# Optimization experiments

Measured on AMD Instinct MI355X. Metric: run time of the kernel, lower is better.

Reference implementation:

```python
import jax, jax.numpy as jnp
import numpy as np

DIM = 512
HID = DIM // 4        # cross-attention inner dim
MLP_HID = int(DIM * 2.0)
EPS = 1e-5


def _xavier(key, shape):
    fan_in, fan_out = shape[0], shape[1]
    limit = float(np.sqrt(6.0 / (fan_in + fan_out)))
    return jax.random.uniform(key, shape, jnp.float32, -limit, limit)


def setup_inputs() -> dict:
    key = jax.random.key(0)
    ks = jax.random.split(key, 12)
    n, v = 8, 2048
    x = jax.random.normal(ks[0], (n, v, DIM), jnp.float32)
    y = jax.random.normal(ks[1], (n, v, DIM), jnp.float32)
    Wq = _xavier(ks[2], (DIM, HID))
    Wk = _xavier(ks[3], (DIM, HID))
    Wv = _xavier(ks[4], (DIM, DIM))
    gamma = jnp.ones((DIM,), jnp.float32)
    beta = jnp.zeros((DIM,), jnp.float32)
    # nn.Linear default init: U(-1/sqrt(fan_in), 1/sqrt(fan_in))
    b1lim = 1.0 / np.sqrt(DIM)
    W1 = jax.random.uniform(ks[5], (DIM, MLP_HID), jnp.float32, -b1lim, b1lim)
    b1 = jax.random.uniform(ks[6], (MLP_HID,), jnp.float32, -b1lim, b1lim)
    b2lim = 1.0 / np.sqrt(MLP_HID)
    W2 = jax.random.uniform(ks[7], (MLP_HID, DIM), jnp.float32, -b2lim, b2lim)
    b2 = jax.random.uniform(ks[8], (DIM,), jnp.float32, -b2lim, b2lim)
    return {"x": x, "y": y, "Wq": Wq, "Wk": Wk, "Wv": Wv,
            "gamma": gamma, "beta": beta, "W1": W1, "b1": b1, "W2": W2, "b2": b2}


def _layernorm(x, gamma, beta):
    mu = jnp.mean(x, axis=-1, keepdims=True)
    var = jnp.var(x, axis=-1, keepdims=True)
    return (x - mu) * jax.lax.rsqrt(var + EPS) * gamma + beta


def reference(x, y, Wq, Wk, Wv, gamma, beta, W1, b1, W2, b2):
    scale = HID ** (-0.5)
    q = jnp.einsum('nvc,co->nvo', x, Wq)          # [n, q, HID]
    k = jnp.einsum('nvc,co->nvo', y, Wk)          # [n, k, HID]
    v = jnp.einsum('nvc,co->nvo', y, Wv)          # [n, k, DIM]
    attn = jax.nn.softmax(jnp.einsum('nqc,nkc->nqk', q, k) * scale, axis=-1)
    x = x + jnp.einsum('nqk,nkc->nqc', attn, v)   # residual + attention
    h = _layernorm(x, gamma, beta)
    h = jax.nn.gelu(h @ W1 + b1, approximate=False) @ W2 + b2
    return x + h
```

## Files before the change

### kernel.cpp

```cpp
#include <hip/hip_runtime.h>
#include <cstddef>
#include <cstdint>

typedef __attribute__((ext_vector_type(8))) short short8;
typedef __attribute__((ext_vector_type(4))) short s16x4;
typedef __attribute__((ext_vector_type(4))) float f32x4;
typedef __attribute__((ext_vector_type(16))) float f32x16;

#define GLOAD_LDS16(gp, lp) __builtin_amdgcn_global_load_lds( \
    (const __attribute__((address_space(1))) void*)(gp),      \
    (__attribute__((address_space(3))) void*)(lp), 16, 0, 0)

__device__ __forceinline__ short f2bf(float f) {
    union { float f; unsigned u; } v; v.f = f;
    unsigned r = v.u + 0x7fffu + ((v.u >> 16) & 1u);
    return (short)(r >> 16);
}

__global__ __launch_bounds__(256) void prep_kernel(
    const float* __restrict__ Wq, const float* __restrict__ Wk,
    const float* __restrict__ Wv, const float* __restrict__ W1,
    const float* __restrict__ W2,
    short* WqT, short* WkT, short* WvT, short* W1T, short* W2T)
{
    __shared__ short tile[64][68];
    int b2 = blockIdx.x;
    const float* in; short* out; int R, C;
    if (b2 < 16)       { in = Wq; out = WqT; R = 512;  C = 128; }
    else if (b2 < 32)  { in = Wk; out = WkT; R = 512;  C = 128;  b2 -= 16; }
    else if (b2 < 96)  { in = Wv; out = WvT; R = 512;  C = 512;  b2 -= 32; }
    else if (b2 < 224) { in = W1; out = W1T; R = 512;  C = 1024; b2 -= 96; }
    else               { in = W2; out = W2T; R = 1024; C = 512;  b2 -= 224; }
    int nx = C >> 6;
    int r0 = (b2 / nx) * 64, c0 = (b2 % nx) * 64;
    int t = threadIdx.x, tr = t >> 6, tc = t & 63;
#pragma unroll
    for (int i = 0; i < 16; ++i) {
        int r = i * 4 + tr;
        tile[r][tc] = f2bf(in[(size_t)(r0 + r) * C + (c0 + tc)]);
    }
    __syncthreads();
#pragma unroll
    for (int i = 0; i < 16; ++i) {
        int r = i * 4 + tr;
        out[(size_t)(c0 + r) * R + (r0 + tc)] = tile[tc][r];
    }
}

__global__ __launch_bounds__(256, 3) void proj_gemm(
    const float* __restrict__ x, const float* __restrict__ y,
    const short* __restrict__ WqT, const short* __restrict__ WkT,
    const short* __restrict__ WvT,
    short* __restrict__ qbf, short* __restrict__ kbff, short* __restrict__ vbf)
{
    __shared__ short As[128][64];
    __shared__ short Bs[128][64];
    int bid = blockIdx.x;
    const float* A; const short* BT; short* outp; int n0, N, mode, mb;
    if (bid < 128)      { A = x; BT = WqT; outp = qbf;  n0 = 0; N = 128; mode = 0; mb = bid; }
    else if (bid < 256) { A = y; BT = WkT; outp = kbff; n0 = 0; N = 128; mode = 0; mb = bid - 128; }
    else { int v2 = bid - 256; A = y; BT = WvT; outp = vbf; n0 = (v2 & 3) << 7; N = 512; mode = 1; mb = v2 >> 2; }
    const int m0 = mb << 7;
    const int K = 512;
    const int t = threadIdx.x, l = t & 63, w = t >> 6;
    const int wm = w >> 1, wn = w & 1;
    const int lo = l & 15, hi = l >> 4;

    f32x4 acc[4][4] = {};
    const int srow = l >> 3;
    const int scg  = (l & 7) ^ (srow & 7);

    for (int kt = 0; kt < K; kt += 64) {
#pragma unroll
        for (int i = 0; i < 4; ++i) {
            int seg = w * 4 + i;
            int row = seg * 8 + srow;
            GLOAD_LDS16(BT + (size_t)(n0 + row) * K + kt + scg * 8, &Bs[seg * 8][0]);
        }
#pragma unroll
        for (int i = 0; i < 4; ++i) {
            int c = i * 256 + t;
            int row = c >> 3, ch = c & 7;
            const float* src = A + (size_t)(m0 + row) * K + kt + ch * 8;
            f32x4 u0 = *(const f32x4*)src;
            f32x4 u1 = *(const f32x4*)(src + 4);
            int d0, d1, d2, d3;
            asm("v_cvt_pk_bf16_f32 %0, %1, %2" : "=v"(d0) : "v"(u0[0]), "v"(u0[1]));
            asm("v_cvt_pk_bf16_f32 %0, %1, %2" : "=v"(d1) : "v"(u0[2]), "v"(u0[3]));
            asm("v_cvt_pk_bf16_f32 %0, %1, %2" : "=v"(d2) : "v"(u1[0]), "v"(u1[1]));
            asm("v_cvt_pk_bf16_f32 %0, %1, %2" : "=v"(d3) : "v"(u1[2]), "v"(u1[3]));
            union { int i[4]; short8 v; } uu;
            uu.i[0] = d0; uu.i[1] = d1; uu.i[2] = d2; uu.i[3] = d3;
            *(short8*)&As[row][((ch ^ (row & 7)) * 8)] = uu.v;
        }
        __syncthreads();
#pragma unroll
        for (int kk = 0; kk < 2; ++kk) {
            short8 af[4], bfv[4];
            const int rc = ((kk * 4 + hi) ^ (lo & 7)) * 8;
#pragma unroll
            for (int mi = 0; mi < 4; ++mi)
                af[mi] = *(const short8*)&As[wm * 64 + mi * 16 + lo][rc];
#pragma unroll
            for (int ni = 0; ni < 4; ++ni)
                bfv[ni] = *(const short8*)&Bs[wn * 64 + ni * 16 + lo][rc];
            __builtin_amdgcn_s_setprio(1);
#pragma unroll
            for (int mi = 0; mi < 4; ++mi)
#pragma unroll
                for (int ni = 0; ni < 4; ++ni)
                    acc[mi][ni] = __builtin_amdgcn_mfma_f32_16x16x32_bf16(
                        af[mi], bfv[ni], acc[mi][ni], 0, 0, 0);
            __builtin_amdgcn_s_setprio(0);
        }
        __syncthreads();
    }

    if (mode == 0) {
#pragma unroll
        for (int mi = 0; mi < 4; ++mi) {
#pragma unroll
            for (int ni = 0; ni < 4; ++ni) {
                int rowb = m0 + wm * 64 + mi * 16 + hi * 4;
                int col  = n0 + wn * 64 + ni * 16 + lo;
                size_t base = ((size_t)(rowb >> 5) * (N >> 4) + (col >> 4)) * 512
                            + ((col & 15) >> 3) * 256 + (rowb & 31) * 8 + (col & 7);
#pragma unroll
                for (int r = 0; r < 4; ++r)
                    outp[base + r * 8] = f2bf(acc[mi][ni][r]);
            }
        }
    } else {
#pragma unroll
        for (int mi = 0; mi < 4; ++mi) {
#pragma unroll
            for (int ni = 0; ni < 4; ++ni) {
                int rowb = m0 + wm * 64 + mi * 16 + hi * 4;
                int col  = n0 + wn * 64 + ni * 16 + lo;
                size_t base = ((size_t)(rowb >> 4) * (N >> 5) + (col >> 5)) * 512
                            + ((rowb & 15) >> 3) * 256 + (col & 31) * 8 + (rowb & 7);
                s16x4 pk;
#pragma unroll
                for (int r = 0; r < 4; ++r) pk[r] = f2bf(acc[mi][ni][r]);
                *(s16x4*)(outp + base) = pk;
            }
        }
    }
}

template<int EPI>
__global__ __launch_bounds__(256, 3) void gemm_kernel(
    const short* __restrict__ A, const short* __restrict__ BT, void* outv,
    const float* __restrict__ bias, const float* __restrict__ resid,
    int N, int K)
{
    __shared__ short As[128][64];
    __shared__ short Bs[128][64];
    int bid = blockIdx.x;
    const int cpx = gridDim.x >> 3;
    bid = (bid & 7) * cpx + (bid >> 3);
    const int nb = N >> 7;
    const int m0 = (bid / nb) << 7;
    const int n0 = (bid % nb) << 7;
    const int t = threadIdx.x, l = t & 63, w = t >> 6;
    const int wm = w >> 1, wn = w & 1;
    const int lo = l & 15, hi = l >> 4;

    f32x4 acc[4][4] = {};
    const int srow = l >> 3;
    const int scg  = (l & 7) ^ (srow & 7);

    for (int kt = 0; kt < K; kt += 64) {
#pragma unroll
        for (int i = 0; i < 4; ++i) {
            int seg = w * 4 + i;
            int row = seg * 8 + srow;
            GLOAD_LDS16(A + (size_t)(m0 + row) * K + kt + scg * 8, &As[seg * 8][0]);
        }
#pragma unroll
        for (int i = 0; i < 4; ++i) {
            int seg = w * 4 + i;
            int row = seg * 8 + srow;
            GLOAD_LDS16(BT + (size_t)(n0 + row) * K + kt + scg * 8, &Bs[seg * 8][0]);
        }
        __syncthreads();
#pragma unroll
        for (int kk = 0; kk < 2; ++kk) {
            short8 af[4], bfv[4];
            const int rc = ((kk * 4 + hi) ^ (lo & 7)) * 8;
#pragma unroll
            for (int mi = 0; mi < 4; ++mi)
                af[mi] = *(const short8*)&As[wm * 64 + mi * 16 + lo][rc];
#pragma unroll
            for (int ni = 0; ni < 4; ++ni)
                bfv[ni] = *(const short8*)&Bs[wn * 64 + ni * 16 + lo][rc];
            __builtin_amdgcn_s_setprio(1);
#pragma unroll
            for (int mi = 0; mi < 4; ++mi)
#pragma unroll
                for (int ni = 0; ni < 4; ++ni)
                    acc[mi][ni] = __builtin_amdgcn_mfma_f32_16x16x32_bf16(
                        af[mi], bfv[ni], acc[mi][ni], 0, 0, 0);
            __builtin_amdgcn_s_setprio(0);
        }
        __syncthreads();
    }

#pragma unroll
    for (int mi = 0; mi < 4; ++mi) {
#pragma unroll
        for (int ni = 0; ni < 4; ++ni) {
#pragma unroll
            for (int r = 0; r < 4; ++r) {
                int row = m0 + wm * 64 + mi * 16 + hi * 4 + r;
                int col = n0 + wn * 64 + ni * 16 + lo;
                size_t idx = (size_t)row * N + col;
                float v = acc[mi][ni][r];
                if (EPI == 2) {
                    v += bias[col];
                    v = 0.5f * v * (1.0f + erff(v * 0.70710678118654752f));
                    ((short*)outv)[idx] = f2bf(v);
                } else {
                    v += bias[col] + resid[idx];
                    ((float*)outv)[idx] = v;
                }
            }
        }
    }
}

__global__ __launch_bounds__(512, 1) void flash_kernel(
    const float* __restrict__ x,
    const short* __restrict__ qbf,
    const short* __restrict__ kbff,
    const short* __restrict__ vbf,
    float* __restrict__ xres,
    const float* __restrict__ gamma,
    const float* __restrict__ beta,
    short* __restrict__ hb)
{
    __shared__ short Ps[2][2][8][512];
    __shared__ float lpart[8][32];
    __shared__ float rsum[8][64];
    __shared__ float rsq[8][64];
    __shared__ float murs[2][64];

    const int bid = blockIdx.x;
    const int n = bid & 7;
    const int qtile = bid >> 3;
    const int q0 = qtile << 6;
    const int t = threadIdx.x, l = t & 63, w = t >> 6;
    const int qh = w >> 2, kq = w & 3;
    const int lo5 = l & 31, hi2 = l >> 5;
    const float C1 = 0.08838834764831845f * 1.4426950408889634f;

    short8 qf[8];
    {
        const short* qp = qbf + (((size_t)(n * 64 + qtile * 2 + qh) * 8) << 9) + l * 8;
#pragma unroll
        for (int s = 0; s < 8; ++s) qf[s] = *(const short8*)(qp + (s << 9));
    }

    f32x16 o00 = {}, o01 = {}, o10 = {}, o11 = {};
    float lp = 0.f;

    const short* kb0 = kbff + (((size_t)(n * 64) * 8) << 9);
    const short* vb0 = vbf + ((((size_t)(n * 128)) * 16 + w * 2) << 9);

    short8 preg0, preg1;

    {
        const short* kp = kb0 + (((size_t)kq * 8) << 9) + l * 8;
        short8 kf[8];
#pragma unroll
        for (int s = 0; s < 8; ++s) kf[s] = *(const short8*)(kp + (s << 9));
        f32x16 sa = {};
        __builtin_amdgcn_s_setprio(1);
#pragma unroll
        for (int s = 0; s < 8; ++s)
            sa = __builtin_amdgcn_mfma_f32_32x32x16_bf16(kf[s], qf[s], sa, 0, 0, 0);
        __builtin_amdgcn_s_setprio(0);
        float lsum = 0.f;
#pragma unroll
        for (int r = 0; r < 16; ++r) {
            float p = exp2f(sa[r] * C1);
            sa[r] = p; lsum += p;
        }
        lp = lsum;
        int wq[8], sx[8];
#pragma unroll
        for (int q2 = 0; q2 < 8; ++q2) {
            int a;
            asm("v_cvt_pk_bf16_f32 %0, %1, %2"
                : "=v"(a) : "v"(sa[2 * q2]), "v"(sa[2 * q2 + 1]));
            wq[q2] = a;
        }
#pragma unroll
        for (int q2 = 0; q2 < 8; ++q2) sx[q2] = __shfl_xor(wq[q2], 32);
        union { int i[4]; short8 v; } u0, u1;
        u0.i[0] = hi2 ? sx[2] : wq[0];
        u0.i[1] = hi2 ? sx[3] : wq[1];
        u0.i[2] = hi2 ? wq[2] : sx[0];
        u0.i[3] = hi2 ? wq[3] : sx[1];
        u1.i[0] = hi2 ? sx[6] : wq[4];
        u1.i[1] = hi2 ? sx[7] : wq[5];
        u1.i[2] = hi2 ? wq[6] : sx[4];
        u1.i[3] = hi2 ? wq[7] : sx[5];
        *(short8*)&Ps[0][qh][kq * 2][l * 8]     = u0.v;
        *(short8*)&Ps[0][qh][kq * 2 + 1][l * 8] = u1.v;
    }

    for (int kt2 = 0; kt2 < 16; ++kt2) {
        const bool hn = kt2 < 15;
        const short* vp = vb0 + (((size_t)(kt2 * 128)) << 9) + l * 8;

        short8 kf[8];
        if (hn) {
            const short* kp = kb0 + (((size_t)((kt2 + 1) * 4 + kq) * 8) << 9) + l * 8;
#pragma unroll
            for (int s = 0; s < 8; ++s) kf[s] = *(const short8*)(kp + (s << 9));
        }
        short8 vfa[8];
#pragma unroll
        for (int p = 0; p < 8; ++p)
            vfa[p] = *(const short8*)(vp + (((size_t)((p >> 1) * 16 + (p & 1))) << 9));

        if (hn) {
            f32x16 sa = {};
            __builtin_amdgcn_s_setprio(1);
#pragma unroll
            for (int s = 0; s < 8; ++s)
                sa = __builtin_amdgcn_mfma_f32_32x32x16_bf16(kf[s], qf[s], sa, 0, 0, 0);
            __builtin_amdgcn_s_setprio(0);
            float lsum = 0.f;
#pragma unroll
            for (int r = 0; r < 16; ++r) {
                float p = exp2f(sa[r] * C1);
                sa[r] = p; lsum += p;
            }
            lp += lsum;
            int wq[8], sx[8];
#pragma unroll
            for (int q2 = 0; q2 < 8; ++q2) {
                int a;
                asm("v_cvt_pk_bf16_f32 %0, %1, %2"
                    : "=v"(a) : "v"(sa[2 * q2]), "v"(sa[2 * q2 + 1]));
                wq[q2] = a;
            }
#pragma unroll
            for (int q2 = 0; q2 < 8; ++q2) sx[q2] = __shfl_xor(wq[q2], 32);
            union { int i[4]; short8 v; } u0, u1;
            u0.i[0] = hi2 ? sx[2] : wq[0];
            u0.i[1] = hi2 ? sx[3] : wq[1];
            u0.i[2] = hi2 ? wq[2] : sx[0];
            u0.i[3] = hi2 ? wq[3] : sx[1];
            u1.i[0] = hi2 ? sx[6] : wq[4];
            u1.i[1] = hi2 ? sx[7] : wq[5];
            u1.i[2] = hi2 ? wq[6] : sx[4];
            u1.i[3] = hi2 ? wq[7] : sx[5];
            preg0 = u0.v; preg1 = u1.v;
        }

        __syncthreads();

        short8 vfb[8];
#pragma unroll
        for (int p = 0; p < 8; ++p)
            vfb[p] = *(const short8*)(vp + (((size_t)((4 + (p >> 1)) * 16 + (p & 1))) << 9));

        if (hn) {
            const int nb2 = (kt2 + 1) & 1;
            *(short8*)&Ps[nb2][qh][kq * 2][l * 8]     = preg0;
            *(short8*)&Ps[nb2][qh][kq * 2 + 1][l * 8] = preg1;
        }

        const int pb = kt2 & 1;
        __builtin_amdgcn_s_setprio(1);
#pragma unroll
        for (int ks = 0; ks < 4; ++ks) {
            short8 p0 = *(const short8*)&Ps[pb][0][ks][l * 8];
            short8 p1 = *(const short8*)&Ps[pb][1][ks][l * 8];
            o00 = __builtin_amdgcn_mfma_f32_32x32x16_bf16(p0, vfa[ks * 2 + 0], o00, 0, 0, 0);
            o01 = __builtin_amdgcn_mfma_f32_32x32x16_bf16(p0, vfa[ks * 2 + 1], o01, 0, 0, 0);
            o10 = __builtin_amdgcn_mfma_f32_32x32x16_bf16(p1, vfa[ks * 2 + 0], o10, 0, 0, 0);
            o11 = __builtin_amdgcn_mfma_f32_32x32x16_bf16(p1, vfa[ks * 2 + 1], o11, 0, 0, 0);
        }
#pragma unroll
        for (int ks = 4; ks < 8; ++ks) {
            short8 p0 = *(const short8*)&Ps[pb][0][ks][l * 8];
            short8 p1 = *(const short8*)&Ps[pb][1][ks][l * 8];
            o00 = __builtin_amdgcn_mfma_f32_32x32x16_bf16(p0, vfb[(ks - 4) * 2 + 0], o00, 0, 0, 0);
            o01 = __builtin_amdgcn_mfma_f32_32x32x16_bf16(p0, vfb[(ks - 4) * 2 + 1], o01, 0, 0, 0);
            o10 = __builtin_amdgcn_mfma_f32_32x32x16_bf16(p1, vfb[(ks - 4) * 2 + 0], o10, 0, 0, 0);
            o11 = __builtin_amdgcn_mfma_f32_32x32x16_bf16(p1, vfb[(ks - 4) * 2 + 1], o11, 0, 0, 0);
        }
        __builtin_amdgcn_s_setprio(0);
    }

    float l2 = lp + __shfl_xor(lp, 32);
    if (l < 32) lpart[w][l] = l2;
    __syncthreads();
    float li0 = 1.f / (lpart[0][lo5] + lpart[1][lo5] + lpart[2][lo5] + lpart[3][lo5]);
    float li1 = 1.f / (lpart[4][lo5] + lpart[5][lo5] + lpart[6][lo5] + lpart[7][lo5]);
    const int c0 = w * 64 + lo5;
#pragma unroll
    for (int r = 0; r < 16; ++r) {
        int qr = (r & 3) + 8 * (r >> 2) + 4 * hi2;
        float ir0 = __shfl(li0, qr);
        float ir1 = __shfl(li1, qr);
        size_t b0 = ((size_t)(n * 2048 + q0 + qr) << 9) + c0;
        size_t b1 = ((size_t)(n * 2048 + q0 + 32 + qr) << 9) + c0;
        float v00 = x[b0]      + o00[r] * ir0;
        float v01 = x[b0 + 32] + o01[r] * ir0;
        float v10 = x[b1]      + o10[r] * ir1;
        float v11 = x[b1 + 32] + o11[r] * ir1;
        xres[b0] = v00; xres[b0 + 32] = v01;
        xres[b1] = v10; xres[b1 + 32] = v11;
        o00[r] = v00; o01[r] = v01; o10[r] = v10; o11[r] = v11;
        float s0 = v00 + v01, sq0 = v00 * v00 + v01 * v01;
        float s1 = v10 + v11, sq1 = v10 * v10 + v11 * v11;
#pragma unroll
        for (int mm = 1; mm < 32; mm <<= 1) {
            s0 += __shfl_xor(s0, mm); sq0 += __shfl_xor(sq0, mm);
            s1 += __shfl_xor(s1, mm); sq1 += __shfl_xor(sq1, mm);
        }
        if (lo5 == 0) {
            rsum[w][qr] = s0;      rsq[w][qr] = sq0;
            rsum[w][32 + qr] = s1; rsq[w][32 + qr] = sq1;
        }
    }
    __syncthreads();
    if (t < 64) {
        float s = 0.f, qq = 0.f;
#pragma unroll
        for (int ww = 0; ww < 8; ++ww) { s += rsum[ww][t]; qq += rsq[ww][t]; }
        float mu = s * (1.0f / 512.0f);
        float var = qq * (1.0f / 512.0f) - mu * mu;
        murs[0][t] = mu;
        murs[1][t] = rsqrtf(var + 1e-5f);
    }
    __syncthreads();
    const float g0 = gamma[c0], g1 = gamma[c0 + 32];
    const float e0 = beta[c0],  e1 = beta[c0 + 32];
#pragma unroll
    for (int r = 0; r < 16; ++r) {
        int qr = (r & 3) + 8 * (r >> 2) + 4 * hi2;
        float mu0 = murs[0][qr],      rs0 = murs[1][qr];
        float mu1 = murs[0][32 + qr], rs1 = murs[1][32 + qr];
        size_t h0 = ((size_t)(n * 2048 + q0 + qr) << 9) + c0;
        size_t h1 = ((size_t)(n * 2048 + q0 + 32 + qr) << 9) + c0;
        hb[h0]      = f2bf((o00[r] - mu0) * rs0 * g0 + e0);
        hb[h0 + 32] = f2bf((o01[r] - mu0) * rs0 * g1 + e1);
        hb[h1]      = f2bf((o10[r] - mu1) * rs1 * g0 + e0);
        hb[h1 + 32] = f2bf((o11[r] - mu1) * rs1 * g1 + e1);
    }
}

extern "C" void kernel_launch(void* const* d_in, const int* in_sizes, int n_in,
                              void* d_out, int out_size, void* d_ws, size_t ws_size,
                              hipStream_t stream)
{
    const float* x     = (const float*)d_in[0];
    const float* y     = (const float*)d_in[1];
    const float* Wq    = (const float*)d_in[2];
    const float* Wk    = (const float*)d_in[3];
    const float* Wv    = (const float*)d_in[4];
    const float* gamma = (const float*)d_in[5];
    const float* beta  = (const float*)d_in[6];
    const float* W1    = (const float*)d_in[7];
    const float* b1    = (const float*)d_in[8];
    const float* W2    = (const float*)d_in[9];
    const float* b2    = (const float*)d_in[10];
    float* out = (float*)d_out;

    char* ws = (char*)d_ws;
    size_t off = 0;
    auto alloc = [&](size_t bytes) -> void* {
        void* p = ws + off;
        off += (bytes + 255) & ~(size_t)255;
        return p;
    };
    short* WqT  = (short*)alloc((size_t)128 * 512 * 2);
    short* WkT  = (short*)alloc((size_t)128 * 512 * 2);
    short* WvT  = (short*)alloc((size_t)512 * 512 * 2);
    short* W1T  = (short*)alloc((size_t)1024 * 512 * 2);
    short* W2T  = (short*)alloc((size_t)512 * 1024 * 2);
    short* qbf  = (short*)alloc((size_t)16384 * 128 * 2);
    short* kbff = (short*)alloc((size_t)16384 * 128 * 2);
    short* vbf  = (short*)alloc((size_t)16384 * 512 * 2);
    short* hb   = (short*)alloc((size_t)16384 * 512 * 2);
    short* gb   = (short*)alloc((size_t)16384 * 1024 * 2);

    prep_kernel<<<352, 256, 0, stream>>>(Wq, Wk, Wv, W1, W2,
                                         WqT, WkT, WvT, W1T, W2T);
    proj_gemm<<<768, 256, 0, stream>>>(x, y, WqT, WkT, WvT, qbf, kbff, vbf);
    flash_kernel<<<256, 512, 0, stream>>>(x, qbf, kbff, vbf, out, gamma, beta, hb);
    gemm_kernel<2><<<1024, 256, 0, stream>>>(hb, W1T, gb, b1, nullptr, 1024, 512);
    gemm_kernel<3><<<512,  256, 0, stream>>>(gb, W2T, out, b2, out, 512, 1024);

    (void)in_sizes; (void)n_in; (void)out_size; (void)ws_size;
}
```

Baseline: 169.0 us.

## Use 16 waves per flash block, splitting query halves across wave groups

Grows the flash attention block from 8 to 16 waves. Each group of 8 waves owns one 32-row query half and computes scores for a 256-key tile, so the loop runs 8 iterations instead of 16. Each wave now holds two output accumulators instead of four. Q and K fragments are reloaded from global memory inside the score loop instead of being kept in registers, and V is loaded in chunks. The aim is more waves in flight and less register pressure per wave, at the cost of repeated Q reads and a larger block barrier.

```diff
diff --git a/kernel.cpp b/kernel.cpp
--- a/kernel.cpp
+++ b/kernel.cpp
@@ -229,7 +229,7 @@
     }
 }
 
-__global__ __launch_bounds__(512, 1) void flash_kernel(
+__global__ __launch_bounds__(1024, 1) void flash_kernel(
     const float* __restrict__ x,
     const short* __restrict__ qbf,
     const short* __restrict__ kbff,
@@ -239,10 +239,10 @@
     const float* __restrict__ beta,
     short* __restrict__ hb)
 {
-    __shared__ short Ps[2][2][8][512];
-    __shared__ float lpart[8][32];
-    __shared__ float rsum[8][64];
-    __shared__ float rsq[8][64];
+    __shared__ short Ps[2][2][16][512];
+    __shared__ float lpart[16][32];
+    __shared__ float rsum[16][32];
+    __shared__ float rsq[16][32];
     __shared__ float murs[2][64];
 
     const int bid = blockIdx.x;
@@ -250,36 +250,26 @@
     const int qtile = bid >> 3;
     const int q0 = qtile << 6;
     const int t = threadIdx.x, l = t & 63, w = t >> 6;
-    const int qh = w >> 2, kq = w & 3;
+    const int qh = w >> 3, sub = w & 7;
     const int lo5 = l & 31, hi2 = l >> 5;
     const float C1 = 0.08838834764831845f * 1.4426950408889634f;
 
-    short8 qf[8];
+    const short* qp = qbf + (((size_t)(n * 64 + qtile * 2 + qh) * 8) << 9) + l * 8;
+    const short* kb0 = kbff + (((size_t)(n * 64) * 8) << 9);
+
+    f32x16 o0 = {}, o1 = {};
+    float lp = 0.f;
+    short8 preg0, preg1;
+
     {
-        const short* qp = qbf + (((size_t)(n * 64 + qtile * 2 + qh) * 8) << 9) + l * 8;
-#pragma unroll
-        for (int s = 0; s < 8; ++s) qf[s] = *(const short8*)(qp + (s << 9));
-    }
-
-    f32x16 o00 = {}, o01 = {}, o10 = {}, o11 = {};
-    float lp = 0.f;
-
-    const short* kb0 = kbff + (((size_t)(n * 64) * 8) << 9);
-    const short* vb0 = vbf + ((((size_t)(n * 128)) * 16 + w * 2) << 9);
-
-    short8 preg0, preg1;
-
-    {
-        const short* kp = kb0 + (((size_t)kq * 8) << 9) + l * 8;
-        short8 kf[8];
-#pragma unroll
-        for (int s = 0; s < 8; ++s) kf[s] = *(const short8*)(kp + (s << 9));
+        const short* kp = kb0 + (((size_t)(sub * 8)) << 9) + l * 8;
         f32x16 sa = {};
-        __builtin_amdgcn_s_setprio(1);
-#pragma unroll
-        for (int s = 0; s < 8; ++s)
-            sa = __builtin_amdgcn_mfma_f32_32x32x16_bf16(kf[s], qf[s], sa, 0, 0, 0);
-        __builtin_amdgcn_s_setprio(0);
+#pragma unroll
+        for (int s = 0; s < 8; ++s) {
+            short8 kf = *(const short8*)(kp + ((size_t)s << 9));
+            short8 qv = *(const short8*)(qp + ((size_t)s << 9));
+            sa = __builtin_amdgcn_mfma_f32_32x32x16_bf16(kf, qv, sa, 0, 0, 0);
+        }
         float lsum = 0.f;
 #pragma unroll
         for (int r = 0; r < 16; ++r) {
@@ -306,31 +296,23 @@
         u1.i[1] = hi2 ? sx[7] : wq[5];
         u1.i[2] = hi2 ? wq[6] : sx[4];
         u1.i[3] = hi2 ? wq[7] : sx[5];
-        *(short8*)&Ps[0][qh][kq * 2][l * 8]     = u0.v;
-        *(short8*)&Ps[0][qh][kq * 2 + 1][l * 8] = u1.v;
-    }
-
-    for (int kt2 = 0; kt2 < 16; ++kt2) {
-        const bool hn = kt2 < 15;
-        const short* vp = vb0 + (((size_t)(kt2 * 128)) << 9) + l * 8;
-
-        short8 kf[8];
+        *(short8*)&Ps[0][qh][sub * 2][l * 8]     = u0.v;
+        *(short8*)&Ps[0][qh][sub * 2 + 1][l * 8] = u1.v;
+    }
+
+    for (int kt2 = 0; kt2 < 8; ++kt2) {
+        const bool hn = kt2 < 7;
+
         if (hn) {
-            const short* kp = kb0 + (((size_t)((kt2 + 1) * 4 + kq) * 8) << 9) + l * 8;
-#pragma unroll
-            for (int s = 0; s < 8; ++s) kf[s] = *(const short8*)(kp + (s << 9));
-        }
-        short8 vfa[8];
-#pragma unroll
-        for (int p = 0; p < 8; ++p)
-            vfa[p] = *(const short8*)(vp + (((size_t)((p >> 1) * 16 + (p & 1))) << 9));
-
-        if (hn) {
+            const short* kp = kb0 + (((size_t)(((kt2 + 1) * 8 + sub) * 8)) << 9) + l * 8;
             f32x16 sa = {};
             __builtin_amdgcn_s_setprio(1);
 #pragma unroll
-            for (int s = 0; s < 8; ++s)
-                sa = __builtin_amdgcn_mfma_f32_32x32x16_bf16(kf[s], qf[s], sa, 0, 0, 0);
+            for (int s = 0; s < 8; ++s) {
+                short8 kf = *(const short8*)(kp + ((size_t)s << 9));
+                short8 qv = *(const short8*)(qp + ((size_t)s << 9));
+                sa = __builtin_amdgcn_mfma_f32_32x32x16_bf16(kf, qv, sa, 0, 0, 0);
+            }
             __builtin_amdgcn_s_setprio(0);
             float lsum = 0.f;
 #pragma unroll
@@ -363,77 +345,68 @@
 
         __syncthreads();
 
-        short8 vfb[8];
-#pragma unroll
-        for (int p = 0; p < 8; ++p)
-            vfb[p] = *(const short8*)(vp + (((size_t)((4 + (p >> 1)) * 16 + (p & 1))) << 9));
-
         if (hn) {
             const int nb2 = (kt2 + 1) & 1;
-            *(short8*)&Ps[nb2][qh][kq * 2][l * 8]     = preg0;
-            *(short8*)&Ps[nb2][qh][kq * 2 + 1][l * 8] = preg1;
+            *(short8*)&Ps[nb2][qh][sub * 2][l * 8]     = preg0;
+            *(short8*)&Ps[nb2][qh][sub * 2 + 1][l * 8] = preg1;
         }
 
         const int pb = kt2 & 1;
-        __builtin_amdgcn_s_setprio(1);
-#pragma unroll
-        for (int ks = 0; ks < 4; ++ks) {
-            short8 p0 = *(const short8*)&Ps[pb][0][ks][l * 8];
-            short8 p1 = *(const short8*)&Ps[pb][1][ks][l * 8];
-            o00 = __builtin_amdgcn_mfma_f32_32x32x16_bf16(p0, vfa[ks * 2 + 0], o00, 0, 0, 0);
-            o01 = __builtin_amdgcn_mfma_f32_32x32x16_bf16(p0, vfa[ks * 2 + 1], o01, 0, 0, 0);
-            o10 = __builtin_amdgcn_mfma_f32_32x32x16_bf16(p1, vfa[ks * 2 + 0], o10, 0, 0, 0);
-            o11 = __builtin_amdgcn_mfma_f32_32x32x16_bf16(p1, vfa[ks * 2 + 1], o11, 0, 0, 0);
-        }
-#pragma unroll
-        for (int ks = 4; ks < 8; ++ks) {
-            short8 p0 = *(const short8*)&Ps[pb][0][ks][l * 8];
-            short8 p1 = *(const short8*)&Ps[pb][1][ks][l * 8];
-            o00 = __builtin_amdgcn_mfma_f32_32x32x16_bf16(p0, vfb[(ks - 4) * 2 + 0], o00, 0, 0, 0);
-            o01 = __builtin_amdgcn_mfma_f32_32x32x16_bf16(p0, vfb[(ks - 4) * 2 + 1], o01, 0, 0, 0);
-            o10 = __builtin_amdgcn_mfma_f32_32x32x16_bf16(p1, vfb[(ks - 4) * 2 + 0], o10, 0, 0, 0);
-            o11 = __builtin_amdgcn_mfma_f32_32x32x16_bf16(p1, vfb[(ks - 4) * 2 + 1], o11, 0, 0, 0);
-        }
-        __builtin_amdgcn_s_setprio(0);
+        const short* vp = vbf + ((((size_t)(n * 128 + kt2 * 16) * 16) + sub * 2) << 9) + l * 8;
+#pragma unroll
+        for (int ch = 0; ch < 4; ++ch) {
+            short8 pa[4], vf[8];
+#pragma unroll
+            for (int j = 0; j < 4; ++j) {
+                int ks = ch * 4 + j;
+                pa[j]         = *(const short8*)&Ps[pb][qh][ks][l * 8];
+                vf[j * 2]     = *(const short8*)(vp + (((size_t)(ks * 16)) << 9));
+                vf[j * 2 + 1] = *(const short8*)(vp + (((size_t)(ks * 16 + 1)) << 9));
+            }
+            __builtin_amdgcn_s_setprio(1);
+#pragma unroll
+            for (int j = 0; j < 4; ++j) {
+                o0 = __builtin_amdgcn_mfma_f32_32x32x16_bf16(pa[j], vf[j * 2],     o0, 0, 0, 0);
+                o1 = __builtin_amdgcn_mfma_f32_32x32x16_bf16(pa[j], vf[j * 2 + 1], o1, 0, 0, 0);
+            }
+            __builtin_amdgcn_s_setprio(0);
+        }
     }
 
     float l2 = lp + __shfl_xor(lp, 32);
     if (l < 32) lpart[w][l] = l2;
     __syncthreads();
-    float li0 = 1.f / (lpart[0][lo5] + lpart[1][lo5] + lpart[2][lo5] + lpart[3][lo5]);
-    float li1 = 1.f / (lpart[4][lo5] + lpart[5][lo5] + lpart[6][lo5] + lpart[7][lo5]);
-    const int c0 = w * 64 + lo5;
+    float li;
+    {
+        const int b0 = qh * 8;
+        li = 1.f / (lpart[b0][lo5] + lpart[b0 + 1][lo5] + lpart[b0 + 2][lo5] +
+                    lpart[b0 + 3][lo5] + lpart[b0 + 4][lo5] + lpart[b0 + 5][lo5] +
+                    lpart[b0 + 6][lo5] + lpart[b0 + 7][lo5]);
+    }
+    const int c0 = sub * 64 + lo5;
 #pragma unroll
     for (int r = 0; r < 16; ++r) {
         int qr = (r & 3) + 8 * (r >> 2) + 4 * hi2;
-        float ir0 = __shfl(li0, qr);
-        float ir1 = __shfl(li1, qr);
-        size_t b0 = ((size_t)(n * 2048 + q0 + qr) << 9) + c0;
-        size_t b1 = ((size_t)(n * 2048 + q0 + 32 + qr) << 9) + c0;
-        float v00 = x[b0]      + o00[r] * ir0;
-        float v01 = x[b0 + 32] + o01[r] * ir0;
-        float v10 = x[b1]      + o10[r] * ir1;
-        float v11 = x[b1 + 32] + o11[r] * ir1;
-        xres[b0] = v00; xres[b0 + 32] = v01;
-        xres[b1] = v10; xres[b1 + 32] = v11;
-        o00[r] = v00; o01[r] = v01; o10[r] = v10; o11[r] = v11;
-        float s0 = v00 + v01, sq0 = v00 * v00 + v01 * v01;
-        float s1 = v10 + v11, sq1 = v10 * v10 + v11 * v11;
+        float ir = __shfl(li, qr);
+        size_t base = ((size_t)(n * 2048 + q0 + qh * 32 + qr) << 9) + c0;
+        float v0 = x[base]      + o0[r] * ir;
+        float v1 = x[base + 32] + o1[r] * ir;
+        xres[base] = v0; xres[base + 32] = v1;
+        o0[r] = v0; o1[r] = v1;
+        float s = v0 + v1;
+        float sq = v0 * v0 + v1 * v1;
 #pragma unroll
         for (int mm = 1; mm < 32; mm <<= 1) {
-            s0 += __shfl_xor(s0, mm); sq0 += __shfl_xor(sq0, mm);
-            s1 += __shfl_xor(s1, mm); sq1 += __shfl_xor(sq1, mm);
-        }
-        if (lo5 == 0) {
-            rsum[w][qr] = s0;      rsq[w][qr] = sq0;
-            rsum[w][32 + qr] = s1; rsq[w][32 + qr] = sq1;
-        }
+            s += __shfl_xor(s, mm); sq += __shfl_xor(sq, mm);
+        }
+        if (lo5 == 0) { rsum[w][qr] = s; rsq[w][qr] = sq; }
     }
     __syncthreads();
     if (t < 64) {
+        const int bq = (t >> 5) * 8, qr = t & 31;
         float s = 0.f, qq = 0.f;
 #pragma unroll
-        for (int ww = 0; ww < 8; ++ww) { s += rsum[ww][t]; qq += rsq[ww][t]; }
+        for (int k = 0; k < 8; ++k) { s += rsum[bq + k][qr]; qq += rsq[bq + k][qr]; }
         float mu = s * (1.0f / 512.0f);
         float var = qq * (1.0f / 512.0f) - mu * mu;
         murs[0][t] = mu;
@@ -445,14 +418,10 @@
 #pragma unroll
     for (int r = 0; r < 16; ++r) {
         int qr = (r & 3) + 8 * (r >> 2) + 4 * hi2;
-        float mu0 = murs[0][qr],      rs0 = murs[1][qr];
-        float mu1 = murs[0][32 + qr], rs1 = murs[1][32 + qr];
-        size_t h0 = ((size_t)(n * 2048 + q0 + qr) << 9) + c0;
-        size_t h1 = ((size_t)(n * 2048 + q0 + 32 + qr) << 9) + c0;
-        hb[h0]      = f2bf((o00[r] - mu0) * rs0 * g0 + e0);
-        hb[h0 + 32] = f2bf((o01[r] - mu0) * rs0 * g1 + e1);
-        hb[h1]      = f2bf((o10[r] - mu1) * rs1 * g0 + e0);
-        hb[h1 + 32] = f2bf((o11[r] - mu1) * rs1 * g1 + e1);
+        float mu = murs[0][qh * 32 + qr], rs = murs[1][qh * 32 + qr];
+        size_t base = ((size_t)(n * 2048 + q0 + qh * 32 + qr) << 9) + c0;
+        hb[base]      = f2bf((o0[r] - mu) * rs * g0 + e0);
+        hb[base + 32] = f2bf((o1[r] - mu) * rs * g1 + e1);
     }
 }
 
@@ -494,7 +463,7 @@
     prep_kernel<<<352, 256, 0, stream>>>(Wq, Wk, Wv, W1, W2,
                                          WqT, WkT, WvT, W1T, W2T);
     proj_gemm<<<768, 256, 0, stream>>>(x, y, WqT, WkT, WvT, qbf, kbff, vbf);
-    flash_kernel<<<256, 512, 0, stream>>>(x, qbf, kbff, vbf, out, gamma, beta, hb);
+    flash_kernel<<<256, 1024, 0, stream>>>(x, qbf, kbff, vbf, out, gamma, beta, hb);
     gemm_kernel<2><<<1024, 256, 0, stream>>>(hb, W1T, gb, b1, nullptr, 1024, 512);
     gemm_kernel<3><<<512,  256, 0, stream>>>(gb, W2T, out, b2, out, 512, 1024);
 
```

After: 180.7 us. +6.9%, slower.
